# Kernel tuning notes

Hardware: AMD Instinct MI355X
Metric: run time of the kernel (lower is better)

## Reference

```python
import jax, jax.numpy as jnp
import numpy as np

NEG_SLOPE = 0.2


def _gat_conv(x, src, dst, W, a_src, a_dst, num_nodes):
    """PyG-style GATConv (single linear for src/dst, softmax over dst neighborhoods).
    x: [N, F_in]; W: [F_in, H*C]; a_src/a_dst: [H, C]. Returns [N, H, C]."""
    H, C = a_src.shape
    h = (x @ W).reshape(num_nodes, H, C)                       # [N, H, C]
    alpha_src = jnp.einsum('nhc,hc->nh', h, a_src)             # [N, H]
    alpha_dst = jnp.einsum('nhc,hc->nh', h, a_dst)             # [N, H]
    e = alpha_src[src] + alpha_dst[dst]                        # [E, H]
    e = jax.nn.leaky_relu(e, NEG_SLOPE)
    # segment softmax over destination node
    m = jax.ops.segment_max(e, dst, num_segments=num_nodes)    # [N, H]
    e = jnp.exp(e - m[dst])
    s = jax.ops.segment_sum(e, dst, num_segments=num_nodes)    # [N, H]
    alpha = e / (s[dst] + 1e-16)                               # [E, H]
    msg = h[src] * alpha[:, :, None]                           # [E, H, C]
    return jax.ops.segment_sum(msg, dst, num_segments=num_nodes)


def setup_inputs() -> dict:
    key = jax.random.key(0)
    ks = jax.random.split(key, 10)
    N, E = 50000, 800000
    F_in, HID, H, OUT = 256, 64, 4, 32
    x = jax.random.normal(ks[0], (N, F_in), dtype=jnp.float32)
    edge_index = jax.random.randint(ks[1], (2, E), 0, N, dtype=jnp.int64)
    s1 = 1.0 / np.sqrt(F_in)
    s2 = 1.0 / np.sqrt(HID * H)
    W1 = jax.random.normal(ks[2], (F_in, H * HID), dtype=jnp.float32) * s1
    att_src1 = jax.random.normal(ks[3], (H, HID), dtype=jnp.float32) * s1
    att_dst1 = jax.random.normal(ks[4], (H, HID), dtype=jnp.float32) * s1
    b1 = jnp.zeros((H * HID,), dtype=jnp.float32)
    W2 = jax.random.normal(ks[5], (H * HID, OUT), dtype=jnp.float32) * s2
    att_src2 = jax.random.normal(ks[6], (1, OUT), dtype=jnp.float32) * s2
    att_dst2 = jax.random.normal(ks[7], (1, OUT), dtype=jnp.float32) * s2
    b2 = jnp.zeros((OUT,), dtype=jnp.float32)
    return {"x": x, "edge_index": edge_index,
            "W1": W1, "att_src1": att_src1, "att_dst1": att_dst1, "b1": b1,
            "W2": W2, "att_src2": att_src2, "att_dst2": att_dst2, "b2": b2}


def reference(x, edge_index, W1, att_src1, att_dst1, b1, W2, att_src2, att_dst2, b2):
    N = x.shape[0]
    # PyG GATConv adds self-loops by default
    loops = jnp.arange(N, dtype=edge_index.dtype)
    src = jnp.concatenate([edge_index[0], loops])
    dst = jnp.concatenate([edge_index[1], loops])
    h1 = _gat_conv(x, src, dst, W1, att_src1, att_dst1, N)      # [N, H, HID]
    h1 = h1.reshape(N, -1) + b1                                 # concat heads + bias
    h1 = jax.nn.relu(h1)                                        # dropout = eval no-op
    h2 = _gat_conv(h1, src, dst, W2, att_src2, att_dst2, N)     # [N, 1, OUT]
    out = h2.mean(axis=1) + b2                                  # concat=False -> mean
    return out
```

## Files before the change

### kernel.cpp

```cpp
#include <hip/hip_runtime.h>
#include <hip/hip_fp16.h>
#include <math.h>

#define FIN  256
#define D1   256
#define NHEAD 4
#define HIDC 64
#define DOUT 32
#define NSLOPE 0.2f

typedef __attribute__((ext_vector_type(8))) short short8v;
typedef __attribute__((ext_vector_type(4))) float f32x4;

__device__ __forceinline__ float lrelu(float x) { return x >= 0.f ? x : NSLOPE * x; }

__device__ __forceinline__ void bf16split(float x, unsigned short& h, unsigned short& l) {
  unsigned u = __float_as_uint(x);
  unsigned uh = (u + 0x7fffu + ((u >> 16) & 1u)) & 0xffff0000u;
  h = (unsigned short)(uh >> 16);
  float r = x - __uint_as_float(uh);
  unsigned ur = __float_as_uint(r);
  l = (unsigned short)((ur + 0x7fffu + ((ur >> 16) & 1u)) >> 16);
}

__global__ void zero2_kernel(int* __restrict__ a, int* __restrict__ b, int n) {
  int i = blockIdx.x * blockDim.x + threadIdx.x;
  if (i < n) { a[i] = 0; b[i] = 0; }
}

__global__ void count_kernel(const int* __restrict__ src, const int* __restrict__ dst,
                             int* __restrict__ deg, int E, int N) {
  int i = blockIdx.x * blockDim.x + threadIdx.x;
  if (i < E) {
    atomicAdd(&deg[dst[i]], 1);
  } else if (i < E + N) {
    atomicAdd(&deg[i - E], 1);
  }
}

__global__ __launch_bounds__(1024) void scan_kernel(const int* __restrict__ deg,
                                                    int* __restrict__ row_ptr, int N) {
  __shared__ int sh[1024];
  int t = threadIdx.x;
  int chunk = (N + 1023) / 1024;
  int b = t * chunk;
  int e = min(b + chunk, N);
  int s = 0;
  for (int i = b; i < e; ++i) s += deg[i];
  sh[t] = s;
  __syncthreads();
  for (int off = 1; off < 1024; off <<= 1) {
    int v = sh[t];
    int u = (t >= off) ? sh[t - off] : 0;
    __syncthreads();
    sh[t] = v + u;
    __syncthreads();
  }
  int run = sh[t] - s;
  for (int i = b; i < e; ++i) { run += deg[i]; row_ptr[i + 1] = run; }
  if (t == 0) row_ptr[0] = 0;
}

__global__ void scatter_kernel(const int* __restrict__ src, const int* __restrict__ dst,
                               const int* __restrict__ row_ptr, int* __restrict__ cur,
                               int* __restrict__ col, int E, int N) {
  int i = blockIdx.x * blockDim.x + threadIdx.x;
  int s, d;
  if (i < E) { s = src[i]; d = dst[i]; }
  else if (i < E + N) { s = i - E; d = i - E; }
  else return;
  int pos = row_ptr[d] + atomicAdd(&cur[d], 1);
  col[pos] = s;
}

__global__ __launch_bounds__(256) void splitW1_kernel(const float* __restrict__ W1,
                                                      unsigned short* __restrict__ Wt_hi,
                                                      unsigned short* __restrict__ Wt_lo) {
  int t = blockIdx.x * 256 + threadIdx.x;
  int c = t >> 8, k = t & 255;
  float x = W1[(size_t)k * D1 + c];
  unsigned short h, l;
  bf16split(x, h, l);
  Wt_hi[(size_t)c * FIN + k] = h;
  Wt_lo[(size_t)c * FIN + k] = l;
}

__global__ __launch_bounds__(256) void gemm1_kernel(const float* __restrict__ A,
                                                    const unsigned short* __restrict__ Bt_hi,
                                                    const unsigned short* __restrict__ Bt_lo,
                                                    __half* __restrict__ C, int N) {
  __shared__ unsigned short As_hi[64][40];
  __shared__ unsigned short As_lo[64][40];
  __shared__ unsigned short Bs_hi[256][40];
  __shared__ unsigned short Bs_lo[256][40];
  int t = threadIdx.x;
  int row0 = blockIdx.x * 64;
  int lane = t & 63;
  int col0 = (t >> 6) * 64;
  int frow = lane & 15;
  int fk8  = lane >> 4;

  f32x4 acc[4][4];
#pragma unroll
  for (int i = 0; i < 4; ++i)
#pragma unroll
    for (int j = 0; j < 4; ++j)
#pragma unroll
      for (int q = 0; q < 4; ++q) acc[i][j][q] = 0.f;

  for (int k0 = 0; k0 < 256; k0 += 32) {
    {
      int r = t >> 3;
      int kk = (t & 7) * 4;
#pragma unroll
      for (int rep = 0; rep < 2; ++rep) {
        int rr = r + rep * 32;
        int gr = row0 + rr;
        float4 v = {0.f, 0.f, 0.f, 0.f};
        if (gr < N) v = *(const float4*)&A[(size_t)gr * FIN + k0 + kk];
        unsigned short h0, l0, h1, l1, h2, l2, h3, l3;
        bf16split(v.x, h0, l0); bf16split(v.y, h1, l1);
        bf16split(v.z, h2, l2); bf16split(v.w, h3, l3);
        ushort4 vh = {h0, h1, h2, h3};
        ushort4 vl = {l0, l1, l2, l3};
        *(ushort4*)&As_hi[rr][kk] = vh;
        *(ushort4*)&As_lo[rr][kk] = vl;
      }
    }
    {
#pragma unroll
      for (int q = 0; q < 4; ++q) {
        int4 vh = *(const int4*)&Bt_hi[(size_t)t * FIN + k0 + q * 8];
        int4 vl = *(const int4*)&Bt_lo[(size_t)t * FIN + k0 + q * 8];
        *(int4*)&Bs_hi[t][q * 8] = vh;
        *(int4*)&Bs_lo[t][q * 8] = vl;
      }
    }
    __syncthreads();
    short8v bh[4], bl[4];
#pragma unroll
    for (int ct = 0; ct < 4; ++ct) {
      bh[ct] = *(const short8v*)&Bs_hi[col0 + ct * 16 + frow][fk8 * 8];
      bl[ct] = *(const short8v*)&Bs_lo[col0 + ct * 16 + frow][fk8 * 8];
    }
#pragma unroll
    for (int rt = 0; rt < 4; ++rt) {
      short8v ah = *(const short8v*)&As_hi[rt * 16 + frow][fk8 * 8];
      short8v al = *(const short8v*)&As_lo[rt * 16 + frow][fk8 * 8];
#pragma unroll
      for (int ct = 0; ct < 4; ++ct) {
        acc[rt][ct] = __builtin_amdgcn_mfma_f32_16x16x32_bf16(ah, bh[ct], acc[rt][ct], 0, 0, 0);
        acc[rt][ct] = __builtin_amdgcn_mfma_f32_16x16x32_bf16(ah, bl[ct], acc[rt][ct], 0, 0, 0);
        acc[rt][ct] = __builtin_amdgcn_mfma_f32_16x16x32_bf16(al, bh[ct], acc[rt][ct], 0, 0, 0);
      }
    }
    __syncthreads();
  }
#pragma unroll
  for (int rt = 0; rt < 4; ++rt) {
#pragma unroll
    for (int i = 0; i < 4; ++i) {
      int gr = row0 + rt * 16 + fk8 * 4 + i;
      if (gr < N) {
#pragma unroll
        for (int ct = 0; ct < 4; ++ct)
          C[(size_t)gr * D1 + col0 + ct * 16 + frow] = __float2half(acc[rt][ct][i]);
      }
    }
  }
}

__global__ __launch_bounds__(256) void alpha1_kernel(const __half* __restrict__ h,
                                                     const float* __restrict__ a_src,
                                                     const float* __restrict__ a_dst,
                                                     float* __restrict__ as,
                                                     float* __restrict__ ad, int N) {
  int wid = (blockIdx.x * blockDim.x + threadIdx.x) >> 6;
  if (wid >= N) return;
  int lane = threadIdx.x & 63;
  int2 r = *(const int2*)&h[(size_t)wid * D1 + lane * 4];
  float2 f01 = __half22float2(*(__half2*)&r.x);
  float2 f23 = __half22float2(*(__half2*)&r.y);
  float4 s4 = *(const float4*)&a_src[lane * 4];
  float4 d4 = *(const float4*)&a_dst[lane * 4];
  float ps = f01.x * s4.x + f01.y * s4.y + f23.x * s4.z + f23.y * s4.w;
  float pd = f01.x * d4.x + f01.y * d4.y + f23.x * d4.z + f23.y * d4.w;
#pragma unroll
  for (int off = 8; off >= 1; off >>= 1) {
    ps += __shfl_xor(ps, off);
    pd += __shfl_xor(pd, off);
  }
  int hh = lane >> 4;
  if ((lane & 15) == 0) { as[wid * 4 + hh] = ps; ad[wid * 4 + hh] = pd; }
}

__global__ __launch_bounds__(256) void stats1_kernel(const float* __restrict__ as1,
                                                     const float* __restrict__ ad1,
                                                     const int* __restrict__ row_ptr,
                                                     const int* __restrict__ col,
                                                     float* __restrict__ mx1,
                                                     float* __restrict__ inv1, int N) {
  int t = blockIdx.x * blockDim.x + threadIdx.x;
  if (t >= N * 4) return;
  int n = t >> 2, h = t & 3;
  int beg = row_ptr[n];
  int deg = row_ptr[n + 1] - beg;
  float adh = ad1[t];
  float m = -INFINITY, s = 0.f;
  int cn = col[beg];
  for (int j = 0; j < deg; ++j) {
    int c = cn;
    if (j + 1 < deg) cn = col[beg + j + 1];
    float e = lrelu(as1[(size_t)c * 4 + h] + adh);
    float nm = fmaxf(m, e);
    s = s * expf(m - nm) + expf(e - nm);
    m = nm;
  }
  mx1[t] = m;
  inv1[t] = 1.f / (s + 1e-16f);
}

__global__ __launch_bounds__(256) void agg1_kernel(const __half* __restrict__ hl,
                                                   const float* __restrict__ as1,
                                                   const float* __restrict__ ad1,
                                                   const float* __restrict__ mx1,
                                                   const float* __restrict__ inv1,
                                                   const int* __restrict__ row_ptr,
                                                   const int* __restrict__ col,
                                                   const float* __restrict__ b1,
                                                   float* __restrict__ h1, int N) {
  int wid = (blockIdx.x * blockDim.x + threadIdx.x) >> 6;
  if (wid >= N) return;
  int lane = threadIdx.x & 63;
  int hm = lane >> 4;
  int beg = row_ptr[wid];
  int deg = row_ptr[wid + 1] - beg;
  float adh = ad1[wid * 4 + hm];
  float mh  = mx1[wid * 4 + hm];
  float ih  = inv1[wid * 4 + hm];
  float4 acc = {0.f, 0.f, 0.f, 0.f};
  int j = 0;
  for (; j + 4 <= deg; j += 4) {
    int s0 = col[beg + j + 0];
    int s1 = col[beg + j + 1];
    int s2 = col[beg + j + 2];
    int s3 = col[beg + j + 3];
    float a0 = as1[(size_t)s0 * 4 + hm];
    float a1 = as1[(size_t)s1 * 4 + hm];
    float a2 = as1[(size_t)s2 * 4 + hm];
    float a3 = as1[(size_t)s3 * 4 + hm];
    int2 r0 = *(const int2*)&hl[(size_t)s0 * D1 + lane * 4];
    int2 r1 = *(const int2*)&hl[(size_t)s1 * D1 + lane * 4];
    int2 r2 = *(const int2*)&hl[(size_t)s2 * D1 + lane * 4];
    int2 r3 = *(const int2*)&hl[(size_t)s3 * D1 + lane * 4];
    float w0 = expf(lrelu(a0 + adh) - mh) * ih;
    float w1 = expf(lrelu(a1 + adh) - mh) * ih;
    float w2 = expf(lrelu(a2 + adh) - mh) * ih;
    float w3 = expf(lrelu(a3 + adh) - mh) * ih;
    float2 u, v;
    u = __half22float2(*(__half2*)&r0.x); v = __half22float2(*(__half2*)&r0.y);
    acc.x = fmaf(w0, u.x, acc.x); acc.y = fmaf(w0, u.y, acc.y);
    acc.z = fmaf(w0, v.x, acc.z); acc.w = fmaf(w0, v.y, acc.w);
    u = __half22float2(*(__half2*)&r1.x); v = __half22float2(*(__half2*)&r1.y);
    acc.x = fmaf(w1, u.x, acc.x); acc.y = fmaf(w1, u.y, acc.y);
    acc.z = fmaf(w1, v.x, acc.z); acc.w = fmaf(w1, v.y, acc.w);
    u = __half22float2(*(__half2*)&r2.x); v = __half22float2(*(__half2*)&r2.y);
    acc.x = fmaf(w2, u.x, acc.x); acc.y = fmaf(w2, u.y, acc.y);
    acc.z = fmaf(w2, v.x, acc.z); acc.w = fmaf(w2, v.y, acc.w);
    u = __half22float2(*(__half2*)&r3.x); v = __half22float2(*(__half2*)&r3.y);
    acc.x = fmaf(w3, u.x, acc.x); acc.y = fmaf(w3, u.y, acc.y);
    acc.z = fmaf(w3, v.x, acc.z); acc.w = fmaf(w3, v.y, acc.w);
  }
  for (; j < deg; ++j) {
    int s0 = col[beg + j];
    float a0 = as1[(size_t)s0 * 4 + hm];
    int2 r0 = *(const int2*)&hl[(size_t)s0 * D1 + lane * 4];
    float w0 = expf(lrelu(a0 + adh) - mh) * ih;
    float2 u = __half22float2(*(__half2*)&r0.x);
    float2 v = __half22float2(*(__half2*)&r0.y);
    acc.x = fmaf(w0, u.x, acc.x); acc.y = fmaf(w0, u.y, acc.y);
    acc.z = fmaf(w0, v.x, acc.z); acc.w = fmaf(w0, v.y, acc.w);
  }
  float4 bb = *(const float4*)&b1[lane * 4];
  float4 o;
  o.x = fmaxf(acc.x + bb.x, 0.f);
  o.y = fmaxf(acc.y + bb.y, 0.f);
  o.z = fmaxf(acc.z + bb.z, 0.f);
  o.w = fmaxf(acc.w + bb.w, 0.f);
  *(float4*)&h1[(size_t)wid * D1 + lane * 4] = o;
}

__global__ __launch_bounds__(256) void gemm2_kernel(const float* __restrict__ A,
                                                    const float* __restrict__ B,
                                                    __half* __restrict__ C, int N) {
  __shared__ float ws[256][33];
  __shared__ float xs[32][132];
  int t = threadIdx.x;
#pragma unroll
  for (int j = 0; j < 32; ++j) {
    int idx = j * 256 + t;
    ws[idx >> 5][idx & 31] = B[idx];
  }
  int row0 = blockIdx.x * 128;
  int tx = t & 31, ty = t >> 5;
  float acc[16] = {};
  for (int k0 = 0; k0 < 256; k0 += 32) {
    __syncthreads();
#pragma unroll
    for (int rep = 0; rep < 4; ++rep) {
      int r = (t >> 3) + rep * 32;
      int kk = (t & 7) * 4;
      int gr = row0 + r;
      float4 v = {0.f, 0.f, 0.f, 0.f};
      if (gr < N) v = *(const float4*)&A[(size_t)gr * D1 + k0 + kk];
      xs[kk + 0][r] = v.x; xs[kk + 1][r] = v.y; xs[kk + 2][r] = v.z; xs[kk + 3][r] = v.w;
    }
    __syncthreads();
#pragma unroll
    for (int k = 0; k < 32; ++k) {
      float w = ws[k0 + k][tx];
#pragma unroll
      for (int rq = 0; rq < 4; ++rq) {
        float4 a4 = *(const float4*)&xs[k][ty * 16 + rq * 4];
        acc[rq * 4 + 0] = fmaf(a4.x, w, acc[rq * 4 + 0]);
        acc[rq * 4 + 1] = fmaf(a4.y, w, acc[rq * 4 + 1]);
        acc[rq * 4 + 2] = fmaf(a4.z, w, acc[rq * 4 + 2]);
        acc[rq * 4 + 3] = fmaf(a4.w, w, acc[rq * 4 + 3]);
      }
    }
  }
#pragma unroll
  for (int j = 0; j < 16; ++j) {
    int gr = row0 + ty * 16 + j;
    if (gr < N) C[(size_t)gr * DOUT + tx] = __float2half(acc[j]);
  }
}

__global__ __launch_bounds__(256) void alpha2_kernel(const __half* __restrict__ h2,
                                                     const float* __restrict__ a_src,
                                                     const float* __restrict__ a_dst,
                                                     float* __restrict__ as,
                                                     float* __restrict__ ad, int N) {
  int wid = (blockIdx.x * blockDim.x + threadIdx.x) >> 6;
  int lane = threadIdx.x & 63;
  int n = wid * 2 + (lane >> 5);
  int c = lane & 31;
  float v = (n < N) ? __half2float(h2[(size_t)n * DOUT + c]) : 0.f;
  float ps = v * a_src[c];
  float pd = v * a_dst[c];
#pragma unroll
  for (int off = 16; off >= 1; off >>= 1) {
    ps += __shfl_xor(ps, off);
    pd += __shfl_xor(pd, off);
  }
  if (c == 0 && n < N) { as[n] = ps; ad[n] = pd; }
}

__global__ __launch_bounds__(256) void stats2_kernel(const float* __restrict__ as2,
                                                     const float* __restrict__ ad2,
                                                     const int* __restrict__ row_ptr,
                                                     const int* __restrict__ col,
                                                     float* __restrict__ mx2,
                                                     float* __restrict__ inv2, int N) {
  int n = blockIdx.x * blockDim.x + threadIdx.x;
  if (n >= N) return;
  int beg = row_ptr[n];
  int deg = row_ptr[n + 1] - beg;
  float ad = ad2[n];
  float m = -INFINITY, s = 0.f;
  int cn = col[beg];
  for (int j = 0; j < deg; ++j) {
    int c = cn;
    if (j + 1 < deg) cn = col[beg + j + 1];
    float e = lrelu(as2[c] + ad);
    float nm = fmaxf(m, e);
    s = s * expf(m - nm) + expf(e - nm);
    m = nm;
  }
  mx2[n] = m;
  inv2[n] = 1.f / (s + 1e-16f);
}

__global__ __launch_bounds__(256) void agg2_kernel(const __half* __restrict__ h2,
                                                   const float* __restrict__ as2,
                                                   const float* __restrict__ ad2,
                                                   const float* __restrict__ mx2,
                                                   const float* __restrict__ inv2,
                                                   const int* __restrict__ row_ptr,
                                                   const int* __restrict__ col,
                                                   const float* __restrict__ b2,
                                                   float* __restrict__ out, int N) {
  int wid = (blockIdx.x * blockDim.x + threadIdx.x) >> 6;
  if (wid >= N) return;
  int lane = threadIdx.x & 63;
  int c = lane & 31;
  int beg = row_ptr[wid];
  int deg = row_ptr[wid + 1] - beg;
  float ad = ad2[wid];
  float mh = mx2[wid];
  float ih = inv2[wid];
  float acc = 0.f;
  int j = 0;
  for (; j + 4 <= deg; j += 4) {
    int s0 = col[beg + j + 0];
    int s1 = col[beg + j + 1];
    int s2 = col[beg + j + 2];
    int s3 = col[beg + j + 3];
    float a0 = as2[s0];
    float a1 = as2[s1];
    float a2 = as2[s2];
    float a3 = as2[s3];
    float v0 = __half2float(h2[(size_t)s0 * DOUT + c]);
    float v1 = __half2float(h2[(size_t)s1 * DOUT + c]);
    float v2 = __half2float(h2[(size_t)s2 * DOUT + c]);
    float v3 = __half2float(h2[(size_t)s3 * DOUT + c]);
    float w0 = expf(lrelu(a0 + ad) - mh) * ih;
    float w1 = expf(lrelu(a1 + ad) - mh) * ih;
    float w2 = expf(lrelu(a2 + ad) - mh) * ih;
    float w3 = expf(lrelu(a3 + ad) - mh) * ih;
    acc = fmaf(w0, v0, acc);
    acc = fmaf(w1, v1, acc);
    acc = fmaf(w2, v2, acc);
    acc = fmaf(w3, v3, acc);
  }
  for (; j < deg; ++j) {
    int s0 = col[beg + j];
    float a0 = as2[s0];
    float v0 = __half2float(h2[(size_t)s0 * DOUT + c]);
    float w0 = expf(lrelu(a0 + ad) - mh) * ih;
    acc = fmaf(w0, v0, acc);
  }
  if (lane < 32) out[(size_t)wid * DOUT + c] = acc + b2[c];
}

extern "C" void kernel_launch(void* const* d_in, const int* in_sizes, int n_in,
                              void* d_out, int out_size, void* d_ws, size_t ws_size,
                              hipStream_t stream) {
  const float* x     = (const float*)d_in[0];
  const int*   ei    = (const int*)d_in[1];
  const float* W1    = (const float*)d_in[2];
  const float* asrc1 = (const float*)d_in[3];
  const float* adst1 = (const float*)d_in[4];
  const float* b1    = (const float*)d_in[5];
  const float* W2    = (const float*)d_in[6];
  const float* asrc2 = (const float*)d_in[7];
  const float* adst2 = (const float*)d_in[8];
  const float* b2    = (const float*)d_in[9];

  const int N = in_sizes[0] / FIN;
  const int E = in_sizes[1] / 2;
  const int ET = E + N;
  const int* src = ei;
  const int* dst = ei + E;

  char* base = (char*)d_ws;
  size_t off = 0;
  auto alloc = [&](size_t bytes) -> void* {
    void* p = base + off;
    off = (off + bytes + 255) & ~(size_t)255;
    return p;
  };
  int* row_ptr = (int*)alloc((size_t)(N + 1) * 4);
  int* deg     = (int*)alloc((size_t)N * 4);
  int* cur     = (int*)alloc((size_t)N * 4);
  int* col     = (int*)alloc((size_t)ET * 4);
  float* as1   = (float*)alloc((size_t)N * 4 * 4);
  float* ad1   = (float*)alloc((size_t)N * 4 * 4);
  float* mx1   = (float*)alloc((size_t)N * 4 * 4);
  float* inv1  = (float*)alloc((size_t)N * 4 * 4);
  float* as2   = (float*)alloc((size_t)N * 4);
  float* ad2   = (float*)alloc((size_t)N * 4);
  float* mx2   = (float*)alloc((size_t)N * 4);
  float* inv2  = (float*)alloc((size_t)N * 4);
  unsigned short* Wt_hi = (unsigned short*)alloc((size_t)FIN * D1 * 2);
  unsigned short* Wt_lo = (unsigned short*)alloc((size_t)FIN * D1 * 2);
  __half* hl1  = (__half*)alloc((size_t)N * D1 * 2);
  float* h1    = (float*)alloc((size_t)N * D1 * 4);
  __half* h2   = hl1;
  float* out   = (float*)d_out;

  hipLaunchKernelGGL(zero2_kernel, dim3((N + 255) / 256), dim3(256), 0, stream, deg, cur, N);
  hipLaunchKernelGGL(count_kernel, dim3((ET + 255) / 256), dim3(256), 0, stream, src, dst, deg, E, N);
  hipLaunchKernelGGL(splitW1_kernel, dim3(FIN * D1 / 256), dim3(256), 0, stream, W1, Wt_hi, Wt_lo);
  hipLaunchKernelGGL(scan_kernel, dim3(1), dim3(1024), 0, stream, deg, row_ptr, N);
  hipLaunchKernelGGL(scatter_kernel, dim3((ET + 255) / 256), dim3(256), 0, stream, src, dst, row_ptr, cur, col, E, N);

  hipLaunchKernelGGL(gemm1_kernel, dim3((N + 63) / 64), dim3(256), 0, stream, x, Wt_hi, Wt_lo, hl1, N);
  hipLaunchKernelGGL(alpha1_kernel, dim3((N + 3) / 4), dim3(256), 0, stream, hl1, asrc1, adst1, as1, ad1, N);
  hipLaunchKernelGGL(stats1_kernel, dim3((N * 4 + 255) / 256), dim3(256), 0, stream, as1, ad1, row_ptr, col, mx1, inv1, N);
  hipLaunchKernelGGL(agg1_kernel, dim3((N + 3) / 4), dim3(256), 0, stream, hl1, as1, ad1, mx1, inv1, row_ptr, col, b1, h1, N);

  hipLaunchKernelGGL(gemm2_kernel, dim3((N + 127) / 128), dim3(256), 0, stream, h1, W2, h2, N);
  hipLaunchKernelGGL(alpha2_kernel, dim3((N + 7) / 8), dim3(256), 0, stream, h2, asrc2, adst2, as2, ad2, N);
  hipLaunchKernelGGL(stats2_kernel, dim3((N + 255) / 256), dim3(256), 0, stream, as2, ad2, row_ptr, col, mx2, inv2, N);
  hipLaunchKernelGGL(agg2_kernel, dim3((N + 3) / 4), dim3(256), 0, stream, h2, as2, ad2, mx2, inv2, row_ptr, col, b2, out, N);
}
```

Baseline: 492.4 us.

## Replace single-block degree scan with three-pass multi-block prefix scan

The CSR row-pointer scan previously ran in one 1024-thread block, with each thread serially walking a chunk of about 49 degrees using strided, uncoalesced loads. It is now split into per-block reductions, a single-block scan of the block sums, and a per-block scan with vectorized int4 loads and wavefront shuffles. This spreads the scan across many CUs and coalesces memory access, at the cost of two extra kernel launches.

```diff
diff --git a/kernel.cpp b/kernel.cpp
--- a/kernel.cpp
+++ b/kernel.cpp
@@ -8,6 +8,7 @@
 #define HIDC 64
 #define DOUT 32
 #define NSLOPE 0.2f
+#define SCHUNK 2048
 
 typedef __attribute__((ext_vector_type(8))) short short8v;
 typedef __attribute__((ext_vector_type(4))) float f32x4;
@@ -38,27 +39,81 @@
   }
 }
 
-__global__ __launch_bounds__(1024) void scan_kernel(const int* __restrict__ deg,
-                                                    int* __restrict__ row_ptr, int N) {
+__global__ __launch_bounds__(256) void scan1_kernel(const int* __restrict__ deg,
+                                                    int* __restrict__ bsum, int N) {
+  int b = blockIdx.x, t = threadIdx.x;
+  int base = b * SCHUNK + t * 8;
+  int s = 0;
+  if (base + 8 <= N) {
+    int4 a = *(const int4*)&deg[base];
+    int4 c = *(const int4*)&deg[base + 4];
+    s = a.x + a.y + a.z + a.w + c.x + c.y + c.z + c.w;
+  } else {
+#pragma unroll
+    for (int i = 0; i < 8; ++i) if (base + i < N) s += deg[base + i];
+  }
+  int lane = t & 63, w = t >> 6;
+#pragma unroll
+  for (int off = 32; off >= 1; off >>= 1) s += __shfl_down(s, off);
+  __shared__ int sh[4];
+  if (lane == 0) sh[w] = s;
+  __syncthreads();
+  if (t == 0) bsum[b] = sh[0] + sh[1] + sh[2] + sh[3];
+}
+
+__global__ __launch_bounds__(1024) void scan2_kernel(int* __restrict__ bsum, int nb) {
   __shared__ int sh[1024];
   int t = threadIdx.x;
-  int chunk = (N + 1023) / 1024;
-  int b = t * chunk;
-  int e = min(b + chunk, N);
-  int s = 0;
-  for (int i = b; i < e; ++i) s += deg[i];
-  sh[t] = s;
+  sh[t] = (t < nb) ? bsum[t] : 0;
   __syncthreads();
   for (int off = 1; off < 1024; off <<= 1) {
-    int v = sh[t];
     int u = (t >= off) ? sh[t - off] : 0;
     __syncthreads();
-    sh[t] = v + u;
+    sh[t] += u;
     __syncthreads();
   }
-  int run = sh[t] - s;
-  for (int i = b; i < e; ++i) { run += deg[i]; row_ptr[i + 1] = run; }
-  if (t == 0) row_ptr[0] = 0;
+  if (t < nb) bsum[t] = sh[t];
+}
+
+__global__ __launch_bounds__(256) void scan3_kernel(const int* __restrict__ deg,
+                                                    const int* __restrict__ bsum,
+                                                    int* __restrict__ row_ptr, int N) {
+  int b = blockIdx.x, t = threadIdx.x;
+  int base = b * SCHUNK + t * 8;
+  int vals[8];
+  if (base + 8 <= N) {
+    int4 a = *(const int4*)&deg[base];
+    int4 c = *(const int4*)&deg[base + 4];
+    vals[0] = a.x; vals[1] = a.y; vals[2] = a.z; vals[3] = a.w;
+    vals[4] = c.x; vals[5] = c.y; vals[6] = c.z; vals[7] = c.w;
+  } else {
+#pragma unroll
+    for (int i = 0; i < 8; ++i) vals[i] = (base + i < N) ? deg[base + i] : 0;
+  }
+  int s = 0;
+#pragma unroll
+  for (int i = 0; i < 8; ++i) { s += vals[i]; vals[i] = s; }
+  int lane = t & 63, w = t >> 6;
+  int inc = s;
+#pragma unroll
+  for (int off = 1; off < 64; off <<= 1) {
+    int u = __shfl_up(inc, off);
+    if (lane >= off) inc += u;
+  }
+  __shared__ int wsum[4];
+  if (lane == 63) wsum[w] = inc;
+  __syncthreads();
+  int woff = 0;
+#pragma unroll
+  for (int i = 0; i < 4; ++i) if (i < w) woff += wsum[i];
+  int excl = woff + inc - s;
+  int offbase = (b ? bsum[b - 1] : 0) + excl;
+#pragma unroll
+  for (int i = 0; i < 8; ++i) {
+    int idx = base + i;
+    if (idx < N) row_ptr[idx + 1] = offbase + vals[i];
+  }
+  if (b == 0 && t == 0) row_ptr[0] = 0;
 }
 
 __global__ void scatter_kernel(const int* __restrict__ src, const int* __restrict__ dst,
@@ -452,6 +507,7 @@
   const int ET = E + N;
   const int* src = ei;
   const int* dst = ei + E;
+  const int NB = (N + SCHUNK - 1) / SCHUNK;
 
   char* base = (char*)d_ws;
   size_t off = 0;
@@ -464,6 +520,7 @@
   int* deg     = (int*)alloc((size_t)N * 4);
   int* cur     = (int*)alloc((size_t)N * 4);
   int* col     = (int*)alloc((size_t)ET * 4);
+  int* bsum    = (int*)alloc((size_t)1024 * 4);
   float* as1   = (float*)alloc((size_t)N * 4 * 4);
   float* ad1   = (float*)alloc((size_t)N * 4 * 4);
   float* mx1   = (float*)alloc((size_t)N * 4 * 4);
@@ -482,7 +539,9 @@
   hipLaunchKernelGGL(zero2_kernel, dim3((N + 255) / 256), dim3(256), 0, stream, deg, cur, N);
   hipLaunchKernelGGL(count_kernel, dim3((ET + 255) / 256), dim3(256), 0, stream, src, dst, deg, E, N);
   hipLaunchKernelGGL(splitW1_kernel, dim3(FIN * D1 / 256), dim3(256), 0, stream, W1, Wt_hi, Wt_lo);
-  hipLaunchKernelGGL(scan_kernel, dim3(1), dim3(1024), 0, stream, deg, row_ptr, N);
+  hipLaunchKernelGGL(scan1_kernel, dim3(NB), dim3(256), 0, stream, deg, bsum, N);
+  hipLaunchKernelGGL(scan2_kernel, dim3(1), dim3(1024), 0, stream, bsum, NB);
+  hipLaunchKernelGGL(scan3_kernel, dim3(NB), dim3(256), 0, stream, deg, bsum, row_ptr, N);
   hipLaunchKernelGGL(scatter_kernel, dim3((ET + 255) / 256), dim3(256), 0, stream, src, dst, row_ptr, cur, col, E, N);
 
   hipLaunchKernelGGL(gemm1_kernel, dim3((N + 63) / 64), dim3(256), 0, stream, x, Wt_hi, Wt_lo, hl1, N);
```

After: 410.9 us. 1.2x faster.
